# Performance work log

Measured on AMD Instinct MI355X. Metric: run time of the kernel, lower is better.

Reference implementation:

```python
import jax, jax.numpy as jnp
import numpy as np

B, V, T = 1024, 50000, 50  # batch, n_items, max tail length

def setup_inputs() -> dict:
    key = jax.random.key(0)
    k1, k2, k3, k4 = jax.random.split(key, 4)
    output = jax.random.normal(k1, (B, V), dtype=jnp.float32)
    target = jax.random.randint(k2, (B,), 0, V, dtype=jnp.int32)
    tails = jax.random.randint(k3, (B, T), 0, V, dtype=jnp.int32)
    tail_len = jax.random.randint(k4, (B,), 0, T, dtype=jnp.int32)  # some rows have 0 -> empty tail
    return {"output": output, "target": target, "tails": tails, "tail_len": tail_len}


def reference(output, target, tails, tail_len):
    # output: [B, V] float scores; target: [B] int; tails: [B, T] padded indices; tail_len: [B]
    target_scores = jnp.take_along_axis(output, target[:, None].astype(jnp.int32), axis=1)[:, 0]  # [B]
    exp_out = jnp.exp(output)
    total_exp = jnp.sum(exp_out, axis=1)  # [B]  (torch: sum(exp(output), 1))
    log_pl = target_scores - jnp.log(total_exp)  # [B]

    # --- ragged tail term, vectorized over rows ---
    s = jnp.take_along_axis(output, tails, axis=1)          # [B, T] tail scores
    mask = jnp.arange(T)[None, :] < tail_len[:, None]       # [B, T] valid positions
    es = jnp.where(mask, jnp.exp(s), 0.0)                   # exp of valid tail scores
    above = jnp.sum(jnp.where(mask, s, 0.0), axis=1)        # [B] sum of tail scores
    # remaining mass: total - exp(target) - sum(exp(tail scores))
    others = total_exp - jnp.exp(target_scores) - jnp.sum(es, axis=1)  # [B]

    # torch flips the valid tail then cumsums exp; with padding at the end,
    # flipping the full padded row puts (zero-contribution) pads first, so the
    # cumsum at valid positions matches the valid-only reversed cumsum.
    fe = es[:, ::-1]                                        # [B, T]
    fmask = mask[:, ::-1]
    c = jnp.cumsum(fe, axis=1)                              # [B, T]
    lg = jnp.log(c + others[:, None])
    below_sum = jnp.sum(jnp.where(fmask, lg, 0.0), axis=1)  # [B]
    tail_term = jnp.where(tail_len > 0, above - below_sum, 0.0)  # rows with empty tail skipped

    neg_like = -(log_pl + tail_term)                        # [B]
    return neg_like
```

## Files before the change

### kernel.cpp

```cpp
#include <hip/hip_runtime.h>

#define BB 1024
#define VV 50000
#define TT 50
#define Q4 3125

__global__ __launch_bounds__(256) void expsum_partial_kernel(
    const float* __restrict__ output,
    float*       __restrict__ partials)
{
    const int blk = blockIdx.x;
    const int row = blk >> 2;
    const int q   = blk & 3;
    const int tid = threadIdx.x;
    const float4* __restrict__ p =
        (const float4*)(output + (size_t)row * VV) + q * Q4;

    float4 v[12];
    #pragma unroll
    for (int u = 0; u < 12; ++u) v[u] = p[tid + 256 * u];
    const bool has_tail = tid < (Q4 - 12 * 256);
    float4 vt = make_float4(0.f, 0.f, 0.f, 0.f);
    if (has_tail) vt = p[tid + 256 * 12];

    float s0 = 0.f, s1 = 0.f, s2 = 0.f, s3 = 0.f;
    #pragma unroll
    for (int u = 0; u < 12; ++u) {
        s0 += __expf(v[u].x);
        s1 += __expf(v[u].y);
        s2 += __expf(v[u].z);
        s3 += __expf(v[u].w);
    }
    if (has_tail) {
        s0 += __expf(vt.x);
        s1 += __expf(vt.y);
        s2 += __expf(vt.z);
        s3 += __expf(vt.w);
    }
    float sum = (s0 + s1) + (s2 + s3);

    #pragma unroll
    for (int off = 32; off > 0; off >>= 1)
        sum += __shfl_down(sum, off, 64);

    __shared__ float wsum[4];
    const int lane = tid & 63;
    const int wave = tid >> 6;
    if (lane == 0) wsum[wave] = sum;
    __syncthreads();
    if (tid == 0)
        partials[blk] = (wsum[0] + wsum[1]) + (wsum[2] + wsum[3]);
}

__global__ __launch_bounds__(64) void tail_kernel(
    const float* __restrict__ output,
    const int*   __restrict__ target,
    const int*   __restrict__ tails,
    const int*   __restrict__ tail_len,
    const float* __restrict__ partials,
    float*       __restrict__ out)
{
    const int r   = blockIdx.x;
    const int tid = threadIdx.x;
    const float* __restrict__ row = output + (size_t)r * VV;

    __shared__ float s_s[TT];
    __shared__ float es_s[TT];

    const int L = tail_len[r];
    if (tid < TT) {
        float sv = 0.f, ev = 0.f;
        if (tid < L) {
            sv = row[tails[r * TT + tid]];
            ev = __expf(sv);
        }
        s_s[tid]  = sv;
        es_s[tid] = ev;
    }
    __syncthreads();

    if (tid == 0) {
        const float total =
            (partials[4 * r] + partials[4 * r + 1]) +
            (partials[4 * r + 2] + partials[4 * r + 3]);
        const float ts = row[target[r]];
        const float log_pl = ts - __logf(total);

        float above = 0.f, sum_es = 0.f;
        for (int j = 0; j < L; ++j) {
            above  += s_s[j];
            sum_es += es_s[j];
        }
        const float others = total - __expf(ts) - sum_es;

        float run = 0.f, below = 0.f;
        for (int k = L - 1; k >= 0; --k) {
            run += es_s[k];
            below += __logf(run + others);
        }
        const float tail_term = (L > 0) ? (above - below) : 0.f;
        out[r] = -(log_pl + tail_term);
    }
}

extern "C" void kernel_launch(void* const* d_in, const int* in_sizes, int n_in,
                              void* d_out, int out_size, void* d_ws, size_t ws_size,
                              hipStream_t stream) {
    const float* output   = (const float*)d_in[0];
    const int*   target   = (const int*)d_in[1];
    const int*   tails    = (const int*)d_in[2];
    const int*   tail_len = (const int*)d_in[3];
    float*       out      = (float*)d_out;
    float*       partials = (float*)d_ws;

    expsum_partial_kernel<<<BB * 4, 256, 0, stream>>>(output, partials);
    tail_kernel<<<BB, 64, 0, stream>>>(output, target, tails, tail_len, partials, out);
}
```

Baseline: 286.8 us.

## Fuse exp-sum and tail computation into one 1024-thread block per row

Merges the partial exp-sum kernel and the tail kernel into a single kernel where one 1024-thread block handles a full row. The partials workspace round-trip and the second launch go away, and the tail gathers run on waves 1 onward in parallel with the reduction. In exchange, a single thread still does the serial tail loop after the block reduction. Fewer, larger blocks (1024 instead of 4096) may also hurt memory-level parallelism and occupancy.

```diff
diff --git a/kernel.cpp b/kernel.cpp
--- a/kernel.cpp
+++ b/kernel.cpp
@@ -3,35 +3,39 @@
 #define BB 1024
 #define VV 50000
 #define TT 50
-#define Q4 3125
+#define NTH 1024
+#define N4  12500
+#define FULL_ITERS 12
+#define REM (N4 - FULL_ITERS * NTH)
 
-__global__ __launch_bounds__(256) void expsum_partial_kernel(
+__global__ __launch_bounds__(NTH) void listmle_fused_kernel(
     const float* __restrict__ output,
-    float*       __restrict__ partials)
+    const int*   __restrict__ target,
+    const int*   __restrict__ tails,
+    const int*   __restrict__ tail_len,
+    float*       __restrict__ out)
 {
-    const int blk = blockIdx.x;
-    const int row = blk >> 2;
-    const int q   = blk & 3;
+    const int r   = blockIdx.x;
     const int tid = threadIdx.x;
-    const float4* __restrict__ p =
-        (const float4*)(output + (size_t)row * VV) + q * Q4;
+    const float* __restrict__ row = output + (size_t)r * VV;
+    const float4* __restrict__ p = (const float4*)row;
 
-    float4 v[12];
+    float4 v[FULL_ITERS];
     #pragma unroll
-    for (int u = 0; u < 12; ++u) v[u] = p[tid + 256 * u];
-    const bool has_tail = tid < (Q4 - 12 * 256);
+    for (int u = 0; u < FULL_ITERS; ++u) v[u] = p[tid + NTH * u];
+    const bool has_rem = tid < REM;
     float4 vt = make_float4(0.f, 0.f, 0.f, 0.f);
-    if (has_tail) vt = p[tid + 256 * 12];
+    if (has_rem) vt = p[tid + NTH * FULL_ITERS];
 
     float s0 = 0.f, s1 = 0.f, s2 = 0.f, s3 = 0.f;
     #pragma unroll
-    for (int u = 0; u < 12; ++u) {
+    for (int u = 0; u < FULL_ITERS; ++u) {
         s0 += __expf(v[u].x);
         s1 += __expf(v[u].y);
         s2 += __expf(v[u].z);
         s3 += __expf(v[u].w);
     }
-    if (has_tail) {
+    if (has_rem) {
         s0 += __expf(vt.x);
         s1 += __expf(vt.y);
         s2 += __expf(vt.z);
@@ -43,46 +47,38 @@
     for (int off = 32; off > 0; off >>= 1)
         sum += __shfl_down(sum, off, 64);
 
-    __shared__ float wsum[4];
+    __shared__ float wsum[16];
+    __shared__ float s_s[TT];
+    __shared__ float es_s[TT];
+    __shared__ float total_s;
+
     const int lane = tid & 63;
     const int wave = tid >> 6;
     if (lane == 0) wsum[wave] = sum;
-    __syncthreads();
-    if (tid == 0)
-        partials[blk] = (wsum[0] + wsum[1]) + (wsum[2] + wsum[3]);
-}
-
-__global__ __launch_bounds__(64) void tail_kernel(
-    const float* __restrict__ output,
-    const int*   __restrict__ target,
-    const int*   __restrict__ tails,
-    const int*   __restrict__ tail_len,
-    const float* __restrict__ partials,
-    float*       __restrict__ out)
-{
-    const int r   = blockIdx.x;
-    const int tid = threadIdx.x;
-    const float* __restrict__ row = output + (size_t)r * VV;
-
-    __shared__ float s_s[TT];
-    __shared__ float es_s[TT];
 
     const int L = tail_len[r];
-    if (tid < TT) {
+    if (tid >= 64 && tid < 64 + TT) {
+        const int j = tid - 64;
         float sv = 0.f, ev = 0.f;
-        if (tid < L) {
-            sv = row[tails[r * TT + tid]];
+        if (j < L) {
+            sv = row[tails[r * TT + j]];
             ev = __expf(sv);
         }
-        s_s[tid]  = sv;
-        es_s[tid] = ev;
+        s_s[j]  = sv;
+        es_s[j] = ev;
     }
     __syncthreads();
 
     if (tid == 0) {
-        const float total =
-            (partials[4 * r] + partials[4 * r + 1]) +
-            (partials[4 * r + 2] + partials[4 * r + 3]);
+        float t = 0.f;
+        #pragma unroll
+        for (int w = 0; w < 16; ++w) t += wsum[w];
+        total_s = t;
+    }
+    __syncthreads();
+
+    if (tid == 0) {
+        const float total = total_s;
         const float ts = row[target[r]];
         const float log_pl = ts - __logf(total);
 
@@ -111,8 +107,6 @@
     const int*   tails    = (const int*)d_in[2];
     const int*   tail_len = (const int*)d_in[3];
     float*       out      = (float*)d_out;
-    float*       partials = (float*)d_ws;
 
-    expsum_partial_kernel<<<BB * 4, 256, 0, stream>>>(output, partials);
-    tail_kernel<<<BB, 64, 0, stream>>>(output, target, tails, tail_len, partials, out);
+    listmle_fused_kernel<<<BB, NTH, 0, stream>>>(output, target, tails, tail_len, out);
 }
```

New measurement: 282.9 us. No clear change (-1.4%).
